# Optimization experiments

Measured on AMD Instinct MI355X. Metric: run time of the kernel, lower is better.

The kernel has to match this reference:

```python
import jax, jax.numpy as jnp
import numpy as np

EPS = 1e-6

def _ln(x, g, b):
    m = jnp.mean(x, axis=-1, keepdims=True)
    v = jnp.mean(jnp.square(x - m), axis=-1, keepdims=True)
    return (x - m) * jax.lax.rsqrt(v + EPS) * g + b

def _pw(x, w, b):
    # 1x1 conv == channel matmul. x: [B,H,W,Ci], w: [Ci,Co]
    return jnp.einsum('bhwc,co->bhwo', x, w) + b

def _dw3x3(x, w, b):
    # depthwise 3x3, SAME. x: [B,H,W,C], w: [3,3,1,C]
    c = x.shape[-1]
    y = jax.lax.conv_general_dilated(
        x, w, window_strides=(1, 1), padding='SAME',
        dimension_numbers=('NHWC', 'HWIO', 'NHWC'),
        feature_group_count=c)
    return y + b

def setup_inputs() -> dict:
    key = jax.random.key(0)
    ks = jax.random.split(key, 16)
    B, H, W, C = 8, 256, 256, 64
    hid = C * 2            # channels * expansion
    s = lambda *sh: 0.02
    inp = {
        'x':     jax.random.normal(ks[0], (B, H, W, C), jnp.float32),
        'ln1_g': jnp.ones((C,), jnp.float32),
        'ln1_b': jnp.zeros((C,), jnp.float32),
        'pw1_w': jax.random.normal(ks[1], (C, hid * 2), jnp.float32) * 0.05,
        'pw1_b': jnp.zeros((hid * 2,), jnp.float32),
        'dw_w':  jax.random.normal(ks[2], (3, 3, 1, hid * 2), jnp.float32) * 0.05,
        'dw_b':  jnp.zeros((hid * 2,), jnp.float32),
        'sca_w': jax.random.normal(ks[3], (hid, hid), jnp.float32) * 0.05,
        'sca_b': jnp.zeros((hid,), jnp.float32),
        'pw2_w': jax.random.normal(ks[4], (hid, C), jnp.float32) * 0.05,
        'pw2_b': jnp.zeros((C,), jnp.float32),
        'beta':  jax.random.normal(ks[5], (1, 1, 1, C), jnp.float32) * 0.1,
        'ln2_g': jnp.ones((C,), jnp.float32),
        'ln2_b': jnp.zeros((C,), jnp.float32),
        'pw3_w': jax.random.normal(ks[6], (C, hid * 2), jnp.float32) * 0.05,
        'pw3_b': jnp.zeros((hid * 2,), jnp.float32),
        'pw4_w': jax.random.normal(ks[7], (hid, C), jnp.float32) * 0.05,
        'pw4_b': jnp.zeros((C,), jnp.float32),
        'gamma': jax.random.normal(ks[8], (1, 1, 1, C), jnp.float32) * 0.1,
    }
    return inp

def reference(x, ln1_g, ln1_b, pw1_w, pw1_b, dw_w, dw_b, sca_w, sca_b,
              pw2_w, pw2_b, beta, ln2_g, ln2_b, pw3_w, pw3_b, pw4_w, pw4_b, gamma):
    # ---- stage 1: norm -> pw1 -> dw3x3 -> SimpleGate -> SCA -> pw2 -> scaled residual
    y = _ln(x, ln1_g, ln1_b)
    y = _pw(y, pw1_w, pw1_b)            # [B,H,W,2*hid]
    y = _dw3x3(y, dw_w, dw_b)
    y1, y2 = jnp.split(y, 2, axis=-1)
    y = y1 * y2                          # SimpleGate -> [B,H,W,hid]
    w = jnp.mean(y, axis=(1, 2), keepdims=True)          # GAP [B,1,1,hid]
    w = _pw(w, sca_w, sca_b)             # 1x1 conv on pooled stats
    y = y * w                            # channel attention
    y = _pw(y, pw2_w, pw2_b)             # [B,H,W,C]
    x = x + y * beta
    # ---- stage 2: norm -> pw3 -> SimpleGate -> pw4 -> scaled residual
    z = _ln(x, ln2_g, ln2_b)
    z = _pw(z, pw3_w, pw3_b)             # [B,H,W,2*hid]
    z1, z2 = jnp.split(z, 2, axis=-1)
    z = z1 * z2                          # [B,H,W,hid]
    z = _pw(z, pw4_w, pw4_b)             # [B,H,W,C]
    return x + z * gamma
```

## Files before the change

### kernel.cpp

```cpp
#include <hip/hip_runtime.h>

typedef __attribute__((ext_vector_type(8))) _Float16 f16x8;
typedef __attribute__((ext_vector_type(2))) _Float16 h2;
typedef __attribute__((ext_vector_type(4))) float f32x4;
typedef __attribute__((ext_vector_type(2))) float f32x2;
typedef __attribute__((ext_vector_type(4))) unsigned uint4_t;
typedef __attribute__((ext_vector_type(2))) unsigned uint2_t;

__device__ __forceinline__ h2 pkrtz(float a, float b) {
    return __builtin_bit_cast(h2, __builtin_amdgcn_cvt_pkrtz(a, b));
}
__device__ __forceinline__ unsigned h2u(h2 v) { return __builtin_bit_cast(unsigned, v); }
__device__ __forceinline__ h2 u2h(unsigned u) { return __builtin_bit_cast(h2, u); }
__device__ __forceinline__ short f2h(float f) { return __builtin_bit_cast(short, (_Float16)f); }

#define OFF_W1T 0L
#define OFF_W2T 32768L
#define OFF_W3T 49152L
#define OFF_W4T 81920L
#define OFF_DWH 98304L
#define OFF_DBH 102912L
#define OFF_WATT 103424L
#define OFF_GPART 107520L
#define OFF_T 631808L

__global__ __launch_bounds__(256) void k_prep(
    const float* __restrict__ w1, const float* __restrict__ w2,
    const float* __restrict__ w3, const float* __restrict__ w4,
    const float* __restrict__ dww, const float* __restrict__ dwb,
    short* __restrict__ w1t, short* __restrict__ w2t,
    short* __restrict__ w3t, short* __restrict__ w4t,
    short* __restrict__ dwh, short* __restrict__ dbh)
{
    int id = blockIdx.x * 256 + threadIdx.x;
    if (id < 64 * 256) {
        int ci = id >> 8, co = id & 255;
        w1t[co * 64 + ci] = f2h(w1[id]);
        w3t[co * 64 + ci] = f2h(w3[id]);
    }
    if (id < 128 * 64) {
        int ci = id >> 6, co = id & 63;
        w2t[co * 128 + ci] = f2h(w2[id]);
        w4t[co * 128 + ci] = f2h(w4[id]);
    }
    if (id < 9 * 256) dwh[id] = f2h(dww[id]);
    if (id < 256)     dbh[id] = f2h(dwb[id]);
}

#define UST 136
__global__ __launch_bounds__(256) void k_a(
    const float* __restrict__ x, const float* __restrict__ ln1g, const float* __restrict__ ln1b,
    const short* __restrict__ w1t, const float* __restrict__ b1,
    const short* __restrict__ dwh, const short* __restrict__ dbh,
    short* __restrict__ t)
{
    __shared__ short uh[100 * UST];
    const int blk = blockIdx.x;
    const int cs  = blk & 1;
    const int txy = blk >> 1;
    const int tx  = txy & 31;
    const int ty  = (txy >> 5) & 31;
    const int b   = txy >> 10;
    const int tid = threadIdx.x;
    const int lane = tid & 63;
    const int wave = tid >> 6;
    const int m    = lane & 15;
    const int quad = lane >> 4;

    for (int tt = wave; tt < 7; tt += 4) {
        int p  = tt * 16 + m;
        int hy = (p * 205) >> 11;
        int hx = p - hy * 10;
        int gy = ty * 8 + hy - 1, gx = tx * 8 + hx - 1;
        bool pin = (p < 100);
        bool img = pin && gy >= 0 && gy < 256 && gx >= 0 && gx < 256;

        f16x8 a0 = {0,0,0,0,0,0,0,0}, a1 = {0,0,0,0,0,0,0,0};
        if (img) {
            const float* xr = x + ((long)((b * 256 + gy) * 256 + gx)) * 64;
            f32x4 f0 = *(const f32x4*)(xr + quad * 8);
            f32x4 f1 = *(const f32x4*)(xr + quad * 8 + 4);
            f32x4 f2 = *(const f32x4*)(xr + 32 + quad * 8);
            f32x4 f3 = *(const f32x4*)(xr + 32 + quad * 8 + 4);
            float s  = (f0[0]+f0[1]+f0[2]+f0[3]) + (f1[0]+f1[1]+f1[2]+f1[3])
                     + (f2[0]+f2[1]+f2[2]+f2[3]) + (f3[0]+f3[1]+f3[2]+f3[3]);
            float s2 = (f0[0]*f0[0]+f0[1]*f0[1]+f0[2]*f0[2]+f0[3]*f0[3])
                     + (f1[0]*f1[0]+f1[1]*f1[1]+f1[2]*f1[2]+f1[3]*f1[3])
                     + (f2[0]*f2[0]+f2[1]*f2[1]+f2[2]*f2[2]+f2[3]*f2[3])
                     + (f3[0]*f3[0]+f3[1]*f3[1]+f3[2]*f3[2]+f3[3]*f3[3]);
            s  += __shfl_xor(s, 16);  s  += __shfl_xor(s, 32);
            s2 += __shfl_xor(s2, 16); s2 += __shfl_xor(s2, 32);
            float mean = s * 0.015625f;
            float var  = s2 * 0.015625f - mean * mean;
            float rs   = rsqrtf(var + 1e-6f);
            float mrs  = mean * rs;
            f32x4 g0 = *(const f32x4*)(ln1g + quad * 8);
            f32x4 g1 = *(const f32x4*)(ln1g + quad * 8 + 4);
            f32x4 g2 = *(const f32x4*)(ln1g + 32 + quad * 8);
            f32x4 g3 = *(const f32x4*)(ln1g + 32 + quad * 8 + 4);
            f32x4 c0 = *(const f32x4*)(ln1b + quad * 8);
            f32x4 c1 = *(const f32x4*)(ln1b + quad * 8 + 4);
            f32x4 c2 = *(const f32x4*)(ln1b + 32 + quad * 8);
            f32x4 c3 = *(const f32x4*)(ln1b + 32 + quad * 8 + 4);
            uint4_t ra, rb;
#define LNP(va,vb,ga,gb,ca,cb) h2u(pkrtz(((va)*rs - mrs)*(ga) + (ca), ((vb)*rs - mrs)*(gb) + (cb)))
            ra[0] = LNP(f0[0],f0[1],g0[0],g0[1],c0[0],c0[1]);
            ra[1] = LNP(f0[2],f0[3],g0[2],g0[3],c0[2],c0[3]);
            ra[2] = LNP(f1[0],f1[1],g1[0],g1[1],c1[0],c1[1]);
            ra[3] = LNP(f1[2],f1[3],g1[2],g1[3],c1[2],c1[3]);
            rb[0] = LNP(f2[0],f2[1],g2[0],g2[1],c2[0],c2[1]);
            rb[1] = LNP(f2[2],f2[3],g2[2],g2[3],c2[2],c2[3]);
            rb[2] = LNP(f3[0],f3[1],g3[0],g3[1],c3[0],c3[1]);
            rb[3] = LNP(f3[2],f3[3],g3[2],g3[3],c3[2],c3[3]);
#undef LNP
            a0 = __builtin_bit_cast(f16x8, ra);
            a1 = __builtin_bit_cast(f16x8, rb);
        }
#pragma unroll
        for (int cot = 0; cot < 8; ++cot) {
            int cob = (cot < 4) ? (cs * 64 + cot * 16) : (128 + cs * 64 + (cot - 4) * 16);
            f16x8 wlo = __builtin_bit_cast(f16x8, *(const uint4_t*)(w1t + (cob + m) * 64 + quad * 8));
            f16x8 whi = __builtin_bit_cast(f16x8, *(const uint4_t*)(w1t + (cob + m) * 64 + 32 + quad * 8));
            f32x4 acc = {0.f, 0.f, 0.f, 0.f};
            acc = __builtin_amdgcn_mfma_f32_16x16x32_f16(wlo, a0, acc, 0, 0, 0);
            acc = __builtin_amdgcn_mfma_f32_16x16x32_f16(whi, a1, acc, 0, 0, 0);
            if (pin) {
                f32x4 bv = *(const f32x4*)(b1 + cob + quad * 4);
                uint2_t pk;
                pk[0] = img ? h2u(pkrtz(acc[0] + bv[0], acc[1] + bv[1])) : 0u;
                pk[1] = img ? h2u(pkrtz(acc[2] + bv[2], acc[3] + bv[3])) : 0u;
                *(uint2_t*)&uh[p * UST + cot * 16 + quad * 4] = pk;
            }
        }
    }
    __syncthreads();

    const int y = lane >> 3, xx = lane & 7;
    const int cq = wave;
    const int gc0 = cs * 64 + cq * 16;
    const long gpx = ((long)(b * 256 + ty * 8 + y) * 256) + tx * 8 + xx;

    h2 A1[8], A2[8];
#pragma unroll
    for (int j = 0; j < 8; ++j) {
        A1[j] = u2h(0u);
        A2[j] = u2h(0u);
    }
#pragma unroll
    for (int dy = 0; dy < 3; ++dy)
#pragma unroll
    for (int dx = 0; dx < 3; ++dx) {
        int h = (y + dy) * 10 + (xx + dx);
        const uint4_t* u1p = (const uint4_t*)&uh[h * UST + cq * 16];
        const uint4_t* u2p = (const uint4_t*)&uh[h * UST + 64 + cq * 16];
        uint4_t u1l = u1p[0], u1h = u1p[1];
        uint4_t u2l = u2p[0], u2hv = u2p[1];
        const uint4_t* wp = (const uint4_t*)(dwh + (dy * 3 + dx) * 256 + gc0);
        const uint4_t* vp = (const uint4_t*)(dwh + (dy * 3 + dx) * 256 + 128 + gc0);
        uint4_t w1l = wp[0], w1h = wp[1];
        uint4_t w2l = vp[0], w2h = vp[1];
#pragma unroll
        for (int j = 0; j < 4; ++j) {
            A1[j]     += u2h(u1l[j])  * u2h(w1l[j]);
            A1[j + 4] += u2h(u1h[j])  * u2h(w1h[j]);
            A2[j]     += u2h(u2l[j])  * u2h(w2l[j]);
            A2[j + 4] += u2h(u2hv[j]) * u2h(w2h[j]);
        }
    }
    const uint4_t* bp1 = (const uint4_t*)(dbh + gc0);
    const uint4_t* bp2 = (const uint4_t*)(dbh + 128 + gc0);
    uint4_t b1l = bp1[0], b1h = bp1[1];
    uint4_t b2l = bp2[0], b2h = bp2[1];
    uint4_t s0, s1;
#pragma unroll
    for (int j = 0; j < 4; ++j) {
        h2 t0 = (A1[j]     + u2h(b1l[j])) * (A2[j]     + u2h(b2l[j]));
        h2 t1 = (A1[j + 4] + u2h(b1h[j])) * (A2[j + 4] + u2h(b2h[j]));
        s0[j] = h2u(t0);
        s1[j] = h2u(t1);
    }
    *(uint4_t*)(t + gpx * 128 + gc0)     = s0;
    *(uint4_t*)(t + gpx * 128 + gc0 + 8) = s1;
}

__global__ __launch_bounds__(256) void k_red(
    const short* __restrict__ t, float* __restrict__ gpart)
{
    __shared__ float red[256][2];
    const int blk = blockIdx.x;
    const int b  = blk >> 7;
    const int sb = blk & 127;
    const int tid = threadIdx.x;
    const int lane = tid & 63, wave = tid >> 6;
    const short* tb = t + ((long)(b * 65536 + sb * 512)) * 128;
    float s0 = 0.f, s1 = 0.f;
#pragma unroll 4
    for (int it = 0; it < 128; ++it) {
        int p = it * 4 + wave;
        unsigned u = *(const unsigned*)(tb + (long)p * 128 + lane * 2);
        h2 v = u2h(u);
        s0 += (float)v[0];
        s1 += (float)v[1];
    }
    red[tid][0] = s0; red[tid][1] = s1;
    __syncthreads();
    if (tid < 64) {
        float r0 = red[tid][0] + red[tid + 64][0] + red[tid + 128][0] + red[tid + 192][0];
        float r1 = red[tid][1] + red[tid + 64][1] + red[tid + 128][1] + red[tid + 192][1];
        f32x2 rv = {r0, r1};
        *(f32x2*)(gpart + (long)blk * 128 + tid * 2) = rv;
    }
}

__global__ __launch_bounds__(1024) void k_sca2(
    const float* __restrict__ gpart, const float* __restrict__ scaw,
    const float* __restrict__ scab, float* __restrict__ watt)
{
    __shared__ float gl[1024];
    const int tid = threadIdx.x;
    const int b = tid >> 7, c = tid & 127;
    float s = 0.f;
#pragma unroll 8
    for (int i = 0; i < 128; ++i) s += gpart[(long)(b * 128 + i) * 128 + c];
    gl[tid] = s * (1.0f / 65536.0f);
    __syncthreads();
    float acc = scab[c];
    const float* g0 = gl + b * 128;
#pragma unroll 8
    for (int ci = 0; ci < 128; ++ci) acc += g0[ci] * scaw[ci * 128 + c];
    watt[tid] = acc;
}

#define XLST 72
#define ZTST 136
__global__ __launch_bounds__(256) void k_b(
    const short* __restrict__ t, const float* __restrict__ watt,
    const short* __restrict__ w2t, const float* __restrict__ b2,
    const float* __restrict__ x, const float* __restrict__ beta,
    const float* __restrict__ ln2g, const float* __restrict__ ln2b,
    const short* __restrict__ w3t, const float* __restrict__ b3,
    const short* __restrict__ w4t, const float* __restrict__ b4,
    const float* __restrict__ gamma, float* __restrict__ out)
{
    __shared__ short xl[4][16 * XLST];
    __shared__ short zt[4][16 * ZTST];
    const int lane = threadIdx.x & 63;
    const int wave = threadIdx.x >> 6;
    const int m = lane & 15, quad = lane >> 4;
    const long px0 = (long)blockIdx.x * 64 + wave * 16;
    const int b = (int)(px0 >> 16);
    const float* wa = watt + b * 128;

    const short* tr = t + (px0 + m) * 128;
    f16x8 bfr[4];
#pragma unroll
    for (int kh = 0; kh < 4; ++kh) {
        uint4_t tvv = *(const uint4_t*)(tr + kh * 32 + quad * 8);
        f32x4 w0  = *(const f32x4*)(wa + kh * 32 + quad * 8);
        f32x4 w1v = *(const f32x4*)(wa + kh * 32 + quad * 8 + 4);
        uint4_t o;
        o[0] = h2u(u2h(tvv[0]) * pkrtz(w0[0],  w0[1]));
        o[1] = h2u(u2h(tvv[1]) * pkrtz(w0[2],  w0[3]));
        o[2] = h2u(u2h(tvv[2]) * pkrtz(w1v[0], w1v[1]));
        o[3] = h2u(u2h(tvv[3]) * pkrtz(w1v[2], w1v[3]));
        bfr[kh] = __builtin_bit_cast(f16x8, o);
    }
    f32x4 acc2[4];
#pragma unroll
    for (int nt = 0; nt < 4; ++nt) { f32x4 z = {0.f,0.f,0.f,0.f}; acc2[nt] = z; }
#pragma unroll
    for (int nt = 0; nt < 4; ++nt)
#pragma unroll
        for (int kh = 0; kh < 4; ++kh) {
            f16x8 aw = __builtin_bit_cast(f16x8,
                *(const uint4_t*)(w2t + (nt * 16 + m) * 128 + kh * 32 + quad * 8));
            acc2[nt] = __builtin_amdgcn_mfma_f32_16x16x32_f16(aw, bfr[kh], acc2[nt], 0, 0, 0);
        }
    float x1v[4][4];
#pragma unroll
    for (int nt = 0; nt < 4; ++nt) {
        int cob = nt * 16 + quad * 4;
        f32x4 xv = *(const f32x4*)(x + (px0 + m) * 64 + cob);
        f32x4 bb = *(const f32x4*)(b2 + cob);
        f32x4 be = *(const f32x4*)(beta + cob);
#pragma unroll
        for (int r = 0; r < 4; ++r)
            x1v[nt][r] = xv[r] + (acc2[nt][r] + bb[r]) * be[r];
    }
    float s = 0.f, s2 = 0.f;
#pragma unroll
    for (int nt = 0; nt < 4; ++nt)
#pragma unroll
        for (int r = 0; r < 4; ++r) { s += x1v[nt][r]; s2 += x1v[nt][r] * x1v[nt][r]; }
    s  += __shfl_xor(s, 16);  s  += __shfl_xor(s, 32);
    s2 += __shfl_xor(s2, 16); s2 += __shfl_xor(s2, 32);
    float mean = s * 0.015625f;
    float var  = s2 * 0.015625f - mean * mean;
    float rs   = rsqrtf(var + 1e-6f);
    float mrs  = mean * rs;
#pragma unroll
    for (int nt = 0; nt < 4; ++nt) {
        int cob = nt * 16 + quad * 4;
        f32x4 gg = *(const f32x4*)(ln2g + cob);
        f32x4 cc = *(const f32x4*)(ln2b + cob);
        float v0 = (x1v[nt][0] * rs - mrs) * gg[0] + cc[0];
        float v1 = (x1v[nt][1] * rs - mrs) * gg[1] + cc[1];
        float v2 = (x1v[nt][2] * rs - mrs) * gg[2] + cc[2];
        float v3 = (x1v[nt][3] * rs - mrs) * gg[3] + cc[3];
        uint2_t pk;
        pk[0] = h2u(pkrtz(v0, v1));
        pk[1] = h2u(pkrtz(v2, v3));
        *(uint2_t*)&xl[wave][m * XLST + cob] = pk;
    }
    __syncthreads();
    f16x8 xb0 = __builtin_bit_cast(f16x8, *(const uint4_t*)&xl[wave][m * XLST + quad * 8]);
    f16x8 xb1 = __builtin_bit_cast(f16x8, *(const uint4_t*)&xl[wave][m * XLST + 32 + quad * 8]);
#pragma unroll
    for (int pg = 0; pg < 8; ++pg) {
        f32x4 aA = {0.f,0.f,0.f,0.f}, aB = {0.f,0.f,0.f,0.f};
        f16x8 w3a0 = __builtin_bit_cast(f16x8, *(const uint4_t*)(w3t + (pg * 16 + m) * 64 + quad * 8));
        f16x8 w3a1 = __builtin_bit_cast(f16x8, *(const uint4_t*)(w3t + (pg * 16 + m) * 64 + 32 + quad * 8));
        f16x8 w3b0 = __builtin_bit_cast(f16x8, *(const uint4_t*)(w3t + (128 + pg * 16 + m) * 64 + quad * 8));
        f16x8 w3b1 = __builtin_bit_cast(f16x8, *(const uint4_t*)(w3t + (128 + pg * 16 + m) * 64 + 32 + quad * 8));
        aA = __builtin_amdgcn_mfma_f32_16x16x32_f16(w3a0, xb0, aA, 0, 0, 0);
        aA = __builtin_amdgcn_mfma_f32_16x16x32_f16(w3a1, xb1, aA, 0, 0, 0);
        aB = __builtin_amdgcn_mfma_f32_16x16x32_f16(w3b0, xb0, aB, 0, 0, 0);
        aB = __builtin_amdgcn_mfma_f32_16x16x32_f16(w3b1, xb1, aB, 0, 0, 0);
        int cb = pg * 16 + quad * 4;
        f32x4 bA = *(const f32x4*)(b3 + cb);
        f32x4 bB = *(const f32x4*)(b3 + 128 + cb);
        float p0 = (aA[0] + bA[0]) * (aB[0] + bB[0]);
        float p1 = (aA[1] + bA[1]) * (aB[1] + bB[1]);
        float p2 = (aA[2] + bA[2]) * (aB[2] + bB[2]);
        float p3 = (aA[3] + bA[3]) * (aB[3] + bB[3]);
        uint2_t pk;
        pk[0] = h2u(pkrtz(p0, p1));
        pk[1] = h2u(pkrtz(p2, p3));
        *(uint2_t*)&zt[wave][m * ZTST + cb] = pk;
    }
    __syncthreads();
    f16x8 zb[4];
#pragma unroll
    for (int kh = 0; kh < 4; ++kh)
        zb[kh] = __builtin_bit_cast(f16x8, *(const uint4_t*)&zt[wave][m * ZTST + kh * 32 + quad * 8]);
    f32x4 acc4[4];
#pragma unroll
    for (int nt = 0; nt < 4; ++nt) { f32x4 z = {0.f,0.f,0.f,0.f}; acc4[nt] = z; }
#pragma unroll
    for (int nt = 0; nt < 4; ++nt)
#pragma unroll
        for (int kh = 0; kh < 4; ++kh) {
            f16x8 aw = __builtin_bit_cast(f16x8,
                *(const uint4_t*)(w4t + (nt * 16 + m) * 128 + kh * 32 + quad * 8));
            acc4[nt] = __builtin_amdgcn_mfma_f32_16x16x32_f16(aw, zb[kh], acc4[nt], 0, 0, 0);
        }
#pragma unroll
    for (int nt = 0; nt < 4; ++nt) {
        int cob = nt * 16 + quad * 4;
        f32x4 bb = *(const f32x4*)(b4 + cob);
        f32x4 gm = *(const f32x4*)(gamma + cob);
        f32x4 o;
#pragma unroll
        for (int r = 0; r < 4; ++r)
            o[r] = x1v[nt][r] + (acc4[nt][r] + bb[r]) * gm[r];
        *(f32x4*)(out + (px0 + m) * 64 + cob) = o;
    }
}

extern "C" void kernel_launch(void* const* d_in, const int* in_sizes, int n_in,
                              void* d_out, int out_size, void* d_ws, size_t ws_size,
                              hipStream_t stream) {
    (void)in_sizes; (void)n_in; (void)out_size; (void)ws_size;
    const float* x    = (const float*)d_in[0];
    const float* ln1g = (const float*)d_in[1];
    const float* ln1b = (const float*)d_in[2];
    const float* pw1w = (const float*)d_in[3];
    const float* pw1b = (const float*)d_in[4];
    const float* dww  = (const float*)d_in[5];
    const float* dwb  = (const float*)d_in[6];
    const float* scaw = (const float*)d_in[7];
    const float* scab = (const float*)d_in[8];
    const float* pw2w = (const float*)d_in[9];
    const float* pw2b = (const float*)d_in[10];
    const float* beta = (const float*)d_in[11];
    const float* ln2g = (const float*)d_in[12];
    const float* ln2b = (const float*)d_in[13];
    const float* pw3w = (const float*)d_in[14];
    const float* pw3b = (const float*)d_in[15];
    const float* pw4w = (const float*)d_in[16];
    const float* pw4b = (const float*)d_in[17];
    const float* gamma= (const float*)d_in[18];

    char* ws = (char*)d_ws;
    short* w1t = (short*)(ws + OFF_W1T);
    short* w2t = (short*)(ws + OFF_W2T);
    short* w3t = (short*)(ws + OFF_W3T);
    short* w4t = (short*)(ws + OFF_W4T);
    short* dwh = (short*)(ws + OFF_DWH);
    short* dbh = (short*)(ws + OFF_DBH);
    float* watt = (float*)(ws + OFF_WATT);
    float* gpart = (float*)(ws + OFF_GPART);
    short* t   = (short*)(ws + OFF_T);
    float* out = (float*)d_out;

    k_prep<<<64, 256, 0, stream>>>(pw1w, pw2w, pw3w, pw4w, dww, dwb,
                                   w1t, w2t, w3t, w4t, dwh, dbh);
    k_a<<<16384, 256, 0, stream>>>(x, ln1g, ln1b, w1t, pw1b, dwh, dbh, t);
    k_red<<<1024, 256, 0, stream>>>(t, gpart);
    k_sca2<<<1, 1024, 0, stream>>>(gpart, scaw, scab, watt);
    k_b<<<8192, 256, 0, stream>>>(t, watt, w2t, pw2b, x, beta, ln2g, ln2b,
                                  w3t, pw3b, w4t, pw4b, gamma, out);
}
```

Measured before the change: 865.0 us.

## Hoist halo loads in k_a, vectorize GAP reduction, parallelize SCA per batch

The halo stage of k_a now issues the x loads for both of a wave's pixel groups before any LayerNorm or MFMA work, and shares weight and bias loads across the two groups, so memory latency can overlap. k_red is rewritten to read 16-byte vectors with one thread per 8 channels over 256 pixels, across twice as many blocks, and the gpart workspace is enlarged to match. k_sca2 now runs one block per batch instead of a single 1024-thread block. k_b issues its residual x loads up front so they overlap the MFMA work. The trade-off is more live registers in k_a and a larger partial-sum buffer.

```diff
diff --git a/kernel.cpp b/kernel.cpp
--- a/kernel.cpp
+++ b/kernel.cpp
@@ -22,7 +22,7 @@
 #define OFF_DBH 102912L
 #define OFF_WATT 103424L
 #define OFF_GPART 107520L
-#define OFF_T 631808L
+#define OFF_T 1156096L
 
 __global__ __launch_bounds__(256) void k_prep(
     const float* __restrict__ w1, const float* __restrict__ w2,
@@ -67,69 +67,127 @@
     const int m    = lane & 15;
     const int quad = lane >> 4;
 
-    for (int tt = wave; tt < 7; tt += 4) {
-        int p  = tt * 16 + m;
-        int hy = (p * 205) >> 11;
-        int hx = p - hy * 10;
-        int gy = ty * 8 + hy - 1, gx = tx * 8 + hx - 1;
-        bool pin = (p < 100);
-        bool img = pin && gy >= 0 && gy < 256 && gx >= 0 && gx < 256;
-
-        f16x8 a0 = {0,0,0,0,0,0,0,0}, a1 = {0,0,0,0,0,0,0,0};
-        if (img) {
-            const float* xr = x + ((long)((b * 256 + gy) * 256 + gx)) * 64;
-            f32x4 f0 = *(const f32x4*)(xr + quad * 8);
-            f32x4 f1 = *(const f32x4*)(xr + quad * 8 + 4);
-            f32x4 f2 = *(const f32x4*)(xr + 32 + quad * 8);
-            f32x4 f3 = *(const f32x4*)(xr + 32 + quad * 8 + 4);
-            float s  = (f0[0]+f0[1]+f0[2]+f0[3]) + (f1[0]+f1[1]+f1[2]+f1[3])
-                     + (f2[0]+f2[1]+f2[2]+f2[3]) + (f3[0]+f3[1]+f3[2]+f3[3]);
-            float s2 = (f0[0]*f0[0]+f0[1]*f0[1]+f0[2]*f0[2]+f0[3]*f0[3])
-                     + (f1[0]*f1[0]+f1[1]*f1[1]+f1[2]*f1[2]+f1[3]*f1[3])
-                     + (f2[0]*f2[0]+f2[1]*f2[1]+f2[2]*f2[2]+f2[3]*f2[3])
-                     + (f3[0]*f3[0]+f3[1]*f3[1]+f3[2]*f3[2]+f3[3]*f3[3]);
-            s  += __shfl_xor(s, 16);  s  += __shfl_xor(s, 32);
-            s2 += __shfl_xor(s2, 16); s2 += __shfl_xor(s2, 32);
-            float mean = s * 0.015625f;
-            float var  = s2 * 0.015625f - mean * mean;
-            float rs   = rsqrtf(var + 1e-6f);
-            float mrs  = mean * rs;
-            f32x4 g0 = *(const f32x4*)(ln1g + quad * 8);
-            f32x4 g1 = *(const f32x4*)(ln1g + quad * 8 + 4);
-            f32x4 g2 = *(const f32x4*)(ln1g + 32 + quad * 8);
-            f32x4 g3 = *(const f32x4*)(ln1g + 32 + quad * 8 + 4);
-            f32x4 c0 = *(const f32x4*)(ln1b + quad * 8);
-            f32x4 c1 = *(const f32x4*)(ln1b + quad * 8 + 4);
-            f32x4 c2 = *(const f32x4*)(ln1b + 32 + quad * 8);
-            f32x4 c3 = *(const f32x4*)(ln1b + 32 + quad * 8 + 4);
-            uint4_t ra, rb;
+    const int pA = wave * 16 + m;
+    const int pB = pA + 64;
+    const int hyA = (pA * 205) >> 11, hxA = pA - hyA * 10;
+    const int hyB = (pB * 205) >> 11, hxB = pB - hyB * 10;
+    const int gyA = ty * 8 + hyA - 1, gxA = tx * 8 + hxA - 1;
+    const int gyB = ty * 8 + hyB - 1, gxB = tx * 8 + hxB - 1;
+    const bool imgA = gyA >= 0 && gyA < 256 && gxA >= 0 && gxA < 256;
+    const bool imgB = (pB < 100) && gyB >= 0 && gyB < 256 && gxB >= 0 && gxB < 256;
+    const bool aliveB = (wave < 3);
+
+    f32x4 fA[4], fB[4];
+#pragma unroll
+    for (int i = 0; i < 4; ++i) {
+        fA[i] = (f32x4){0.f,0.f,0.f,0.f};
+        fB[i] = (f32x4){0.f,0.f,0.f,0.f};
+    }
+    if (imgA) {
+        const float* xr = x + ((long)((b * 256 + gyA) * 256 + gxA)) * 64 + quad * 8;
+        fA[0] = *(const f32x4*)(xr);      fA[1] = *(const f32x4*)(xr + 4);
+        fA[2] = *(const f32x4*)(xr + 32); fA[3] = *(const f32x4*)(xr + 36);
+    }
+    if (imgB) {
+        const float* xr = x + ((long)((b * 256 + gyB) * 256 + gxB)) * 64 + quad * 8;
+        fB[0] = *(const f32x4*)(xr);      fB[1] = *(const f32x4*)(xr + 4);
+        fB[2] = *(const f32x4*)(xr + 32); fB[3] = *(const f32x4*)(xr + 36);
+    }
+
+    f16x8 a0A = {0,0,0,0,0,0,0,0}, a1A = {0,0,0,0,0,0,0,0};
+    f16x8 a0B = {0,0,0,0,0,0,0,0}, a1B = {0,0,0,0,0,0,0,0};
+
+    if (imgA) {
+        float s  = 0.f, s2 = 0.f;
+#pragma unroll
+        for (int i = 0; i < 4; ++i)
+#pragma unroll
+            for (int r = 0; r < 4; ++r) { s += fA[i][r]; s2 += fA[i][r] * fA[i][r]; }
+        s  += __shfl_xor(s, 16);  s  += __shfl_xor(s, 32);
+        s2 += __shfl_xor(s2, 16); s2 += __shfl_xor(s2, 32);
+        float mean = s * 0.015625f;
+        float var  = s2 * 0.015625f - mean * mean;
+        float rs   = rsqrtf(var + 1e-6f);
+        float mrs  = mean * rs;
+        f32x4 g0 = *(const f32x4*)(ln1g + quad * 8);
+        f32x4 g1 = *(const f32x4*)(ln1g + quad * 8 + 4);
+        f32x4 g2 = *(const f32x4*)(ln1g + 32 + quad * 8);
+        f32x4 g3 = *(const f32x4*)(ln1g + 32 + quad * 8 + 4);
+        f32x4 c0 = *(const f32x4*)(ln1b + quad * 8);
+        f32x4 c1 = *(const f32x4*)(ln1b + quad * 8 + 4);
+        f32x4 c2 = *(const f32x4*)(ln1b + 32 + quad * 8);
+        f32x4 c3 = *(const f32x4*)(ln1b + 32 + quad * 8 + 4);
+        uint4_t ra, rb;
 #define LNP(va,vb,ga,gb,ca,cb) h2u(pkrtz(((va)*rs - mrs)*(ga) + (ca), ((vb)*rs - mrs)*(gb) + (cb)))
-            ra[0] = LNP(f0[0],f0[1],g0[0],g0[1],c0[0],c0[1]);
-            ra[1] = LNP(f0[2],f0[3],g0[2],g0[3],c0[2],c0[3]);
-            ra[2] = LNP(f1[0],f1[1],g1[0],g1[1],c1[0],c1[1]);
-            ra[3] = LNP(f1[2],f1[3],g1[2],g1[3],c1[2],c1[3]);
-            rb[0] = LNP(f2[0],f2[1],g2[0],g2[1],c2[0],c2[1]);
-            rb[1] = LNP(f2[2],f2[3],g2[2],g2[3],c2[2],c2[3]);
-            rb[2] = LNP(f3[0],f3[1],g3[0],g3[1],c3[0],c3[1]);
-            rb[3] = LNP(f3[2],f3[3],g3[2],g3[3],c3[2],c3[3]);
+        ra[0] = LNP(fA[0][0],fA[0][1],g0[0],g0[1],c0[0],c0[1]);
+        ra[1] = LNP(fA[0][2],fA[0][3],g0[2],g0[3],c0[2],c0[3]);
+        ra[2] = LNP(fA[1][0],fA[1][1],g1[0],g1[1],c1[0],c1[1]);
+        ra[3] = LNP(fA[1][2],fA[1][3],g1[2],g1[3],c1[2],c1[3]);
+        rb[0] = LNP(fA[2][0],fA[2][1],g2[0],g2[1],c2[0],c2[1]);
+        rb[1] = LNP(fA[2][2],fA[2][3],g2[2],g2[3],c2[2],c2[3]);
+        rb[2] = LNP(fA[3][0],fA[3][1],g3[0],g3[1],c3[0],c3[1]);
+        rb[3] = LNP(fA[3][2],fA[3][3],g3[2],g3[3],c3[2],c3[3]);
+        a0A = __builtin_bit_cast(f16x8, ra);
+        a1A = __builtin_bit_cast(f16x8, rb);
+    }
+    if (imgB) {
+        float s  = 0.f, s2 = 0.f;
+#pragma unroll
+        for (int i = 0; i < 4; ++i)
+#pragma unroll
+            for (int r = 0; r < 4; ++r) { s += fB[i][r]; s2 += fB[i][r] * fB[i][r]; }
+        s  += __shfl_xor(s, 16);  s  += __shfl_xor(s, 32);
+        s2 += __shfl_xor(s2, 16); s2 += __shfl_xor(s2, 32);
+        float mean = s * 0.015625f;
+        float var  = s2 * 0.015625f - mean * mean;
+        float rs   = rsqrtf(var + 1e-6f);
+        float mrs  = mean * rs;
+        f32x4 g0 = *(const f32x4*)(ln1g + quad * 8);
+        f32x4 g1 = *(const f32x4*)(ln1g + quad * 8 + 4);
+        f32x4 g2 = *(const f32x4*)(ln1g + 32 + quad * 8);
+        f32x4 g3 = *(const f32x4*)(ln1g + 32 + quad * 8 + 4);
+        f32x4 c0 = *(const f32x4*)(ln1b + quad * 8);
+        f32x4 c1 = *(const f32x4*)(ln1b + quad * 8 + 4);
+        f32x4 c2 = *(const f32x4*)(ln1b + 32 + quad * 8);
+        f32x4 c3 = *(const f32x4*)(ln1b + 32 + quad * 8 + 4);
+        uint4_t ra, rb;
+        ra[0] = LNP(fB[0][0],fB[0][1],g0[0],g0[1],c0[0],c0[1]);
+        ra[1] = LNP(fB[0][2],fB[0][3],g0[2],g0[3],c0[2],c0[3]);
+        ra[2] = LNP(fB[1][0],fB[1][1],g1[0],g1[1],c1[0],c1[1]);
+        ra[3] = LNP(fB[1][2],fB[1][3],g1[2],g1[3],c1[2],c1[3]);
+        rb[0] = LNP(fB[2][0],fB[2][1],g2[0],g2[1],c2[0],c2[1]);
+        rb[1] = LNP(fB[2][2],fB[2][3],g2[2],g2[3],c2[2],c2[3]);
+        rb[2] = LNP(fB[3][0],fB[3][1],g3[0],g3[1],c3[0],c3[1]);
+        rb[3] = LNP(fB[3][2],fB[3][3],g3[2],g3[3],c3[2],c3[3]);
 #undef LNP
-            a0 = __builtin_bit_cast(f16x8, ra);
-            a1 = __builtin_bit_cast(f16x8, rb);
+        a0B = __builtin_bit_cast(f16x8, ra);
+        a1B = __builtin_bit_cast(f16x8, rb);
+    }
+
+#pragma unroll
+    for (int cot = 0; cot < 8; ++cot) {
+        const int cob = (cot < 4) ? (cs * 64 + cot * 16) : (128 + cs * 64 + (cot - 4) * 16);
+        const f16x8 wlo = __builtin_bit_cast(f16x8, *(const uint4_t*)(w1t + (cob + m) * 64 + quad * 8));
+        const f16x8 whi = __builtin_bit_cast(f16x8, *(const uint4_t*)(w1t + (cob + m) * 64 + 32 + quad * 8));
+        const f32x4 bv = *(const f32x4*)(b1 + cob + quad * 4);
+        {
+            f32x4 acc = {0.f,0.f,0.f,0.f};
+            acc = __builtin_amdgcn_mfma_f32_16x16x32_f16(wlo, a0A, acc, 0, 0, 0);
+            acc = __builtin_amdgcn_mfma_f32_16x16x32_f16(whi, a1A, acc, 0, 0, 0);
+            uint2_t pk;
+            pk[0] = imgA ? h2u(pkrtz(acc[0] + bv[0], acc[1] + bv[1])) : 0u;
+            pk[1] = imgA ? h2u(pkrtz(acc[2] + bv[2], acc[3] + bv[3])) : 0u;
+            *(uint2_t*)&uh[pA * UST + cot * 16 + quad * 4] = pk;
         }
-#pragma unroll
-        for (int cot = 0; cot < 8; ++cot) {
-            int cob = (cot < 4) ? (cs * 64 + cot * 16) : (128 + cs * 64 + (cot - 4) * 16);
-            f16x8 wlo = __builtin_bit_cast(f16x8, *(const uint4_t*)(w1t + (cob + m) * 64 + quad * 8));
-            f16x8 whi = __builtin_bit_cast(f16x8, *(const uint4_t*)(w1t + (cob + m) * 64 + 32 + quad * 8));
-            f32x4 acc = {0.f, 0.f, 0.f, 0.f};
-            acc = __builtin_amdgcn_mfma_f32_16x16x32_f16(wlo, a0, acc, 0, 0, 0);
-            acc = __builtin_amdgcn_mfma_f32_16x16x32_f16(whi, a1, acc, 0, 0, 0);
-            if (pin) {
-                f32x4 bv = *(const f32x4*)(b1 + cob + quad * 4);
+        if (aliveB) {
+            f32x4 acc = {0.f,0.f,0.f,0.f};
+            acc = __builtin_amdgcn_mfma_f32_16x16x32_f16(wlo, a0B, acc, 0, 0, 0);
+            acc = __builtin_amdgcn_mfma_f32_16x16x32_f16(whi, a1B, acc, 0, 0, 0);
+            if (pB < 100) {
                 uint2_t pk;
-                pk[0] = img ? h2u(pkrtz(acc[0] + bv[0], acc[1] + bv[1])) : 0u;
-                pk[1] = img ? h2u(pkrtz(acc[2] + bv[2], acc[3] + bv[3])) : 0u;
-                *(uint2_t*)&uh[p * UST + cot * 16 + quad * 4] = pk;
+                pk[0] = imgB ? h2u(pkrtz(acc[0] + bv[0], acc[1] + bv[1])) : 0u;
+                pk[1] = imgB ? h2u(pkrtz(acc[2] + bv[2], acc[3] + bv[3])) : 0u;
+                *(uint2_t*)&uh[pB * UST + cot * 16 + quad * 4] = pk;
             }
         }
     }
@@ -186,49 +244,53 @@
 __global__ __launch_bounds__(256) void k_red(
     const short* __restrict__ t, float* __restrict__ gpart)
 {
-    __shared__ float red[256][2];
+    __shared__ float red[16][16][8];
     const int blk = blockIdx.x;
-    const int b  = blk >> 7;
-    const int sb = blk & 127;
     const int tid = threadIdx.x;
-    const int lane = tid & 63, wave = tid >> 6;
-    const short* tb = t + ((long)(b * 65536 + sb * 512)) * 128;
-    float s0 = 0.f, s1 = 0.f;
+    const int cg = tid & 15;
+    const int pr = tid >> 4;
+    const short* tb = t + (long)blk * 256 * 128 + cg * 8;
+    float a0=0,a1=0,a2=0,a3=0,a4=0,a5=0,a6=0,a7=0;
 #pragma unroll 4
-    for (int it = 0; it < 128; ++it) {
-        int p = it * 4 + wave;
-        unsigned u = *(const unsigned*)(tb + (long)p * 128 + lane * 2);
-        h2 v = u2h(u);
-        s0 += (float)v[0];
-        s1 += (float)v[1];
-    }
-    red[tid][0] = s0; red[tid][1] = s1;
-    __syncthreads();
-    if (tid < 64) {
-        float r0 = red[tid][0] + red[tid + 64][0] + red[tid + 128][0] + red[tid + 192][0];
-        float r1 = red[tid][1] + red[tid + 64][1] + red[tid + 128][1] + red[tid + 192][1];
-        f32x2 rv = {r0, r1};
-        *(f32x2*)(gpart + (long)blk * 128 + tid * 2) = rv;
-    }
-}
-
-__global__ __launch_bounds__(1024) void k_sca2(
+    for (int it = 0; it < 16; ++it) {
+        uint4_t u = *(const uint4_t*)(tb + (long)(it * 16 + pr) * 128);
+        h2 v0=u2h(u[0]), v1=u2h(u[1]), v2=u2h(u[2]), v3=u2h(u[3]);
+        a0 += (float)v0[0]; a1 += (float)v0[1]; a2 += (float)v1[0]; a3 += (float)v1[1];
+        a4 += (float)v2[0]; a5 += (float)v2[1]; a6 += (float)v3[0]; a7 += (float)v3[1];
+    }
+    red[pr][cg][0]=a0; red[pr][cg][1]=a1; red[pr][cg][2]=a2; red[pr][cg][3]=a3;
+    red[pr][cg][4]=a4; red[pr][cg][5]=a5; red[pr][cg][6]=a6; red[pr][cg][7]=a7;
+    __syncthreads();
+    if (tid < 128) {
+        int g = tid >> 3, j = tid & 7;
+        float s = 0.f;
+#pragma unroll
+        for (int r = 0; r < 16; ++r) s += red[r][g][j];
+        gpart[(long)blk * 128 + tid] = s;
+    }
+}
+
+__global__ __launch_bounds__(256) void k_sca2(
     const float* __restrict__ gpart, const float* __restrict__ scaw,
     const float* __restrict__ scab, float* __restrict__ watt)
 {
-    __shared__ float gl[1024];
+    __shared__ float gl[256];
+    __shared__ float gn[128];
+    const int b = blockIdx.x;
     const int tid = threadIdx.x;
-    const int b = tid >> 7, c = tid & 127;
+    const int c = tid & 127, half = tid >> 7;
     float s = 0.f;
-#pragma unroll 8
-    for (int i = 0; i < 128; ++i) s += gpart[(long)(b * 128 + i) * 128 + c];
-    gl[tid] = s * (1.0f / 65536.0f);
-    __syncthreads();
-    float acc = scab[c];
-    const float* g0 = gl + b * 128;
-#pragma unroll 8
-    for (int ci = 0; ci < 128; ++ci) acc += g0[ci] * scaw[ci * 128 + c];
-    watt[tid] = acc;
+    const float* gp = gpart + (long)b * 256 * 128 + c;
+    for (int i = half; i < 256; i += 2) s += gp[(long)i * 128];
+    gl[half * 128 + c] = s;
+    __syncthreads();
+    if (tid < 128) gn[c] = (gl[c] + gl[128 + c]) * (1.0f / 65536.0f);
+    __syncthreads();
+    if (tid < 128) {
+        float acc = scab[c];
+        for (int ci = 0; ci < 128; ++ci) acc += gn[ci] * scaw[ci * 128 + c];
+        watt[b * 128 + c] = acc;
+    }
 }
 
 #define XLST 72
@@ -251,6 +313,11 @@
     const int b = (int)(px0 >> 16);
     const float* wa = watt + b * 128;
 
+    f32x4 xv[4];
+#pragma unroll
+    for (int nt = 0; nt < 4; ++nt)
+        xv[nt] = *(const f32x4*)(x + (px0 + m) * 64 + nt * 16 + quad * 4);
+
     const short* tr = t + (px0 + m) * 128;
     f16x8 bfr[4];
 #pragma unroll
@@ -280,12 +347,11 @@
 #pragma unroll
     for (int nt = 0; nt < 4; ++nt) {
         int cob = nt * 16 + quad * 4;
-        f32x4 xv = *(const f32x4*)(x + (px0 + m) * 64 + cob);
         f32x4 bb = *(const f32x4*)(b2 + cob);
         f32x4 be = *(const f32x4*)(beta + cob);
 #pragma unroll
         for (int r = 0; r < 4; ++r)
-            x1v[nt][r] = xv[r] + (acc2[nt][r] + bb[r]) * be[r];
+            x1v[nt][r] = xv[nt][r] + (acc2[nt][r] + bb[r]) * be[r];
     }
     float s = 0.f, s2 = 0.f;
 #pragma unroll
@@ -406,8 +472,8 @@
     k_prep<<<64, 256, 0, stream>>>(pw1w, pw2w, pw3w, pw4w, dww, dwb,
                                    w1t, w2t, w3t, w4t, dwh, dbh);
     k_a<<<16384, 256, 0, stream>>>(x, ln1g, ln1b, w1t, pw1b, dwh, dbh, t);
-    k_red<<<1024, 256, 0, stream>>>(t, gpart);
-    k_sca2<<<1, 1024, 0, stream>>>(gpart, scaw, scab, watt);
+    k_red<<<2048, 256, 0, stream>>>(t, gpart);
+    k_sca2<<<8, 256, 0, stream>>>(gpart, scaw, scab, watt);
     k_b<<<8192, 256, 0, stream>>>(t, watt, w2t, pw2b, x, beta, ln2g, ln2b,
                                   w3t, pw3b, w4t, pw4b, gamma, out);
 }
```

Result: no change. 860.9 us (-0.5%).
